# Kernel optimization log

Measured on AMD Instinct MI355X. Metric: run time of the kernel, lower is better.

## Reference

```python
import jax, jax.numpy as jnp
import numpy as np

N_NODES = 100000


def _mean_agg(x, src, dst, n_nodes):
    # gather source features along edges, segment-sum into destinations, divide by in-degree
    msg = x[src]                                               # [E, D]
    s = jax.ops.segment_sum(msg, dst, num_segments=n_nodes)    # [N, D]
    deg = jax.ops.segment_sum(jnp.ones((src.shape[0],), x.dtype), dst, num_segments=n_nodes)
    return s / jnp.maximum(deg, 1.0)[:, None]


def _sage_layer(x, src, dst, W_self, W_neigh, b, n_nodes):
    h_neigh = _mean_agg(x, src, dst, n_nodes)
    return x @ W_self + h_neigh @ W_neigh + b


def setup_inputs() -> dict:
    key = jax.random.key(0)
    ks = jax.random.split(key, 8)
    in_f, h_f, n_cls = 128, 128, 40
    n_edges = 1600000
    sc = lambda d: 1.0 / np.sqrt(d)
    return {
        "features": jax.random.normal(ks[0], (N_NODES, in_f), dtype=jnp.float32),
        "src": jax.random.randint(ks[1], (n_edges,), 0, N_NODES),
        "dst": jax.random.randint(ks[2], (n_edges,), 0, N_NODES),
        "W1_self": jax.random.normal(ks[3], (in_f, h_f), dtype=jnp.float32) * sc(in_f),
        "W1_neigh": jax.random.normal(ks[4], (in_f, h_f), dtype=jnp.float32) * sc(in_f),
        "b1": jnp.zeros((h_f,), dtype=jnp.float32),
        "W2_self": jax.random.normal(ks[5], (h_f, n_cls), dtype=jnp.float32) * sc(h_f),
        "W2_neigh": jax.random.normal(ks[6], (h_f, n_cls), dtype=jnp.float32) * sc(h_f),
        "b2": jnp.zeros((n_cls,), dtype=jnp.float32),
    }


def reference(features, src, dst, W1_self, W1_neigh, b1, W2_self, W2_neigh, b2):
    h = _sage_layer(features, src, dst, W1_self, W1_neigh, b1, N_NODES)
    h = jax.nn.relu(h)
    h = _sage_layer(h, src, dst, W2_self, W2_neigh, b2, N_NODES)
    return h
```

## Files before the change

kernel.cpp:

```cpp
#include <hip/hip_runtime.h>


typedef __attribute__((ext_vector_type(8))) short bf16x8;
typedef __attribute__((ext_vector_type(4))) float f32x4;

#define BIN_SHIFT 7
#define BIN_SIZE  128
#define NB        256

#define OFF_ROWSTART (1ull << 20)
#define OFF_HIST     (2ull << 20)
#define OFF_SCAN     (3ull << 20)
#define OFF_BSUMS    (4ull << 20)
#define OFF_BOFFS    ((4ull << 20) + (64ull << 10))
#define OFF_PACKED   (5ull << 20)
#define OFF_CSR      (12ull << 20)
#define OFF_W1T      (19ull << 20)
#define OFF_W2T      (20ull << 20)
#define OFF_XB       (21ull << 20)
#define OFF_AGGB     (47ull << 20)
#define OFF_T2LO     (73ull << 20)
#define OFF_T2HI     (80ull << 20)

static __device__ __forceinline__ unsigned short f2b(float f) {
    unsigned int u = __float_as_uint(f);
    u += 0x7fffu + ((u >> 16) & 1u);
    return (unsigned short)(u >> 16);
}
static __device__ __forceinline__ float blo(unsigned int v) { return __uint_as_float(v << 16); }
static __device__ __forceinline__ float bhi(unsigned int v) { return __uint_as_float(v & 0xffff0000u); }


__global__ __launch_bounds__(256) void hist_local(
    const int* __restrict__ dst, int* __restrict__ hist, int E, int nbins) {
    __shared__ int h[1024];
    int b = blockIdx.x, t = threadIdx.x;
    for (int i = t; i < nbins; i += 256) h[i] = 0;
    __syncthreads();
    int chunk = (E + NB - 1) / NB;
    int base = b * chunk;
    int lim = min(base + chunk, E);
    for (int e = base + t; e < lim; e += 256)
        atomicAdd(&h[dst[e] >> BIN_SHIFT], 1);
    __syncthreads();
    for (int i = t; i < nbins; i += 256)
        hist[i * NB + b] = h[i];
}

__global__ void scan1(const int* __restrict__ in, int* __restrict__ tmp,
                      int* __restrict__ bsums, int M) {
    __shared__ int s[256];
    int t = threadIdx.x;
    int i = blockIdx.x * 256 + t;
    int v = (i < M) ? in[i] : 0;
    s[t] = v;
    __syncthreads();
    for (int off = 1; off < 256; off <<= 1) {
        int u = (t >= off) ? s[t - off] : 0;
        __syncthreads();
        s[t] += u;
        __syncthreads();
    }
    if (i < M) tmp[i] = s[t] - v;
    if (t == 255) bsums[blockIdx.x] = s[t];
}

__global__ void scan2(const int* __restrict__ bsums, int* __restrict__ boffs, int nb) {
    __shared__ int s[1024];
    int t = threadIdx.x;
    int v = (t < nb) ? bsums[t] : 0;
    s[t] = v;
    __syncthreads();
    for (int off = 1; off < 1024; off <<= 1) {
        int u = (t >= off) ? s[t - off] : 0;
        __syncthreads();
        s[t] += u;
        __syncthreads();
    }
    if (t < nb) boffs[t] = s[t] - v;
}

__global__ void scan3(int* __restrict__ tmp, const int* __restrict__ boffs, int M) {
    int i = blockIdx.x * 256 + threadIdx.x;
    if (i < M) tmp[i] += boffs[blockIdx.x];
}

__global__ __launch_bounds__(256) void scatter_det(
    const int* __restrict__ src, const int* __restrict__ dst,
    const int* __restrict__ scanned, unsigned int* __restrict__ packed,
    int E, int nbins) {
    __shared__ int cur[1024];
    int b = blockIdx.x, t = threadIdx.x;
    for (int i = t; i < nbins; i += 256) cur[i] = scanned[i * NB + b];
    __syncthreads();
    int chunk = (E + NB - 1) / NB;
    int base = b * chunk;
    int lim = min(base + chunk, E);
    for (int e = base + t; e < lim; e += 256) {
        int d = dst[e];
        int bin = d >> BIN_SHIFT;
        int pos = atomicAdd(&cur[bin], 1);
        packed[pos] = ((unsigned int)(d & (BIN_SIZE - 1)) << 20) | (unsigned int)src[e];
    }
}

__global__ __launch_bounds__(256) void bin_fill(
    const unsigned int* __restrict__ packed, const int* __restrict__ scanned,
    int* __restrict__ row_start, int* __restrict__ csr_src, int N, int nbins, int E) {
    __shared__ int cnt[BIN_SIZE];
    __shared__ int pre[BIN_SIZE];
    __shared__ int ex[BIN_SIZE];
    int b = blockIdx.x;
    int t = threadIdx.x;
    int node0 = b << BIN_SHIFT;
    int beg = scanned[b * NB];
    int end = (b + 1 < nbins) ? scanned[(b + 1) * NB] : E;

    if (t < BIN_SIZE) cnt[t] = 0;
    __syncthreads();
    for (int i = beg + t; i < end; i += 256)
        atomicAdd(&cnt[packed[i] >> 20], 1);
    __syncthreads();
    if (t < BIN_SIZE) pre[t] = cnt[t];
    __syncthreads();
    for (int off = 1; off < BIN_SIZE; off <<= 1) {
        int u = (t < BIN_SIZE && t >= off) ? pre[t - off] : 0;
        __syncthreads();
        if (t < BIN_SIZE) pre[t] += u;
        __syncthreads();
    }
    if (t < BIN_SIZE) {
        ex[t] = pre[t] - cnt[t];
        int node = node0 + t;
        if (node < N) row_start[node] = beg + ex[t];
        cnt[t] = 0;
    }
    if (b == nbins - 1 && t == 0) row_start[N] = E;
    __syncthreads();
    for (int i = beg + t; i < end; i += 256) {
        unsigned int p = packed[i];
        int dl = p >> 20;
        int s = p & 0xFFFFF;
        int ofs = atomicAdd(&cnt[dl], 1);
        csr_src[beg + ex[dl] + ofs] = s;
    }
}


__global__ void cast_bf16(const float* __restrict__ x, unsigned short* __restrict__ xb, int n8) {
    int i = blockIdx.x * blockDim.x + threadIdx.x;
    if (i >= n8) return;
    const float4* p = (const float4*)x + (size_t)i * 2;
    float4 v0 = p[0], v1 = p[1];
    unsigned short o[8];
    o[0] = f2b(v0.x); o[1] = f2b(v0.y); o[2] = f2b(v0.z); o[3] = f2b(v0.w);
    o[4] = f2b(v1.x); o[5] = f2b(v1.y); o[6] = f2b(v1.z); o[7] = f2b(v1.w);
    *(float4*)(xb + (size_t)i * 8) = *(float4*)o;
}

__global__ void prep_weights(const float* __restrict__ W1s, const float* __restrict__ W1n,
                             const float* __restrict__ W2s, const float* __restrict__ W2n,
                             unsigned short* __restrict__ W1t, unsigned short* __restrict__ W2t) {
    int blk = blockIdx.x, k = threadIdx.x;
    if (blk < 128) {
        int c = blk;
        float v = (k < 128) ? W1s[(size_t)k * 128 + c] : W1n[(size_t)(k - 128) * 128 + c];
        W1t[(size_t)c * 256 + k] = f2b(v);
    } else if (k < 128) {
        int c = blk - 128;
        float v = (c < 40) ? W2s[(size_t)k * 40 + c] : W2n[(size_t)k * 40 + (c - 40)];
        W2t[(size_t)c * 128 + k] = f2b(v);
    }
}


__global__ void agg_mean_bf16(const unsigned short* __restrict__ xb,
                              const int* __restrict__ row_start,
                              const int* __restrict__ csr_src,
                              unsigned short* __restrict__ aggb, int N) {
    int wave = (blockIdx.x * blockDim.x + threadIdx.x) >> 6;
    int lane = threadIdx.x & 63;
    if (wave >= N) return;
    int q = lane >> 4;
    int l = lane & 15;
    int beg = row_start[wave], end = row_start[wave + 1];
    const char* xbase = (const char*)xb;
    unsigned loff = (unsigned)l << 4;

    float a0 = 0.f, a1 = 0.f, a2 = 0.f, a3 = 0.f;
    float a4 = 0.f, a5 = 0.f, a6 = 0.f, a7 = 0.f;

    int e = beg;
    for (; e + 16 <= end; e += 16) {
        int eq = e + 4 * q;
        int s0 = csr_src[eq + 0];
        int s1 = csr_src[eq + 1];
        int s2 = csr_src[eq + 2];
        int s3 = csr_src[eq + 3];
        uint4 v0 = *(const uint4*)(xbase + (((unsigned)s0 << 8) + loff));
        uint4 v1 = *(const uint4*)(xbase + (((unsigned)s1 << 8) + loff));
        uint4 v2 = *(const uint4*)(xbase + (((unsigned)s2 << 8) + loff));
        uint4 v3 = *(const uint4*)(xbase + (((unsigned)s3 << 8) + loff));
        a0 += blo(v0.x) + blo(v1.x) + blo(v2.x) + blo(v3.x);
        a1 += bhi(v0.x) + bhi(v1.x) + bhi(v2.x) + bhi(v3.x);
        a2 += blo(v0.y) + blo(v1.y) + blo(v2.y) + blo(v3.y);
        a3 += bhi(v0.y) + bhi(v1.y) + bhi(v2.y) + bhi(v3.y);
        a4 += blo(v0.z) + blo(v1.z) + blo(v2.z) + blo(v3.z);
        a5 += bhi(v0.z) + bhi(v1.z) + bhi(v2.z) + bhi(v3.z);
        a6 += blo(v0.w) + blo(v1.w) + blo(v2.w) + blo(v3.w);
        a7 += bhi(v0.w) + bhi(v1.w) + bhi(v2.w) + bhi(v3.w);
    }
    for (; e + 4 <= end; e += 4) {
        int s = csr_src[e + q];
        uint4 v = *(const uint4*)(xbase + (((unsigned)s << 8) + loff));
        a0 += blo(v.x); a1 += bhi(v.x); a2 += blo(v.y); a3 += bhi(v.y);
        a4 += blo(v.z); a5 += bhi(v.z); a6 += blo(v.w); a7 += bhi(v.w);
    }
    int rem = end - e;
    if (q < rem) {
        int s = csr_src[e + q];
        uint4 v = *(const uint4*)(xbase + (((unsigned)s << 8) + loff));
        a0 += blo(v.x); a1 += bhi(v.x); a2 += blo(v.y); a3 += bhi(v.y);
        a4 += blo(v.z); a5 += bhi(v.z); a6 += blo(v.w); a7 += bhi(v.w);
    }
    a0 += __shfl_xor(a0, 16); a0 += __shfl_xor(a0, 32);
    a1 += __shfl_xor(a1, 16); a1 += __shfl_xor(a1, 32);
    a2 += __shfl_xor(a2, 16); a2 += __shfl_xor(a2, 32);
    a3 += __shfl_xor(a3, 16); a3 += __shfl_xor(a3, 32);
    a4 += __shfl_xor(a4, 16); a4 += __shfl_xor(a4, 32);
    a5 += __shfl_xor(a5, 16); a5 += __shfl_xor(a5, 32);
    a6 += __shfl_xor(a6, 16); a6 += __shfl_xor(a6, 32);
    a7 += __shfl_xor(a7, 16); a7 += __shfl_xor(a7, 32);
    if (q == 0) {
        float inv = 1.0f / fmaxf((float)(end - beg), 1.0f);
        uint4 o;
        o.x = (unsigned int)f2b(a0 * inv) | ((unsigned int)f2b(a1 * inv) << 16);
        o.y = (unsigned int)f2b(a2 * inv) | ((unsigned int)f2b(a3 * inv) << 16);
        o.z = (unsigned int)f2b(a4 * inv) | ((unsigned int)f2b(a5 * inv) << 16);
        o.w = (unsigned int)f2b(a6 * inv) | ((unsigned int)f2b(a7 * inv) << 16);
        *(uint4*)((char*)aggb + (((unsigned)wave << 8) + loff)) = o;
    }
}

__global__ void agg2_add(const unsigned short* __restrict__ t2lo,
                         const unsigned short* __restrict__ t2hi,
                         const int* __restrict__ row_start,
                         const int* __restrict__ csr_src, const float* __restrict__ b2,
                         float* __restrict__ out, int N) {
    int wave = (blockIdx.x * blockDim.x + threadIdx.x) >> 6;
    int lane = threadIdx.x & 63;
    if (wave >= N) return;
    int q = lane >> 4;
    int l = lane & 15;
    int beg = row_start[wave], end = row_start[wave + 1];
    const char* lob = (const char*)t2lo;
    const char* hib = (const char*)t2hi;
    bool isLo = (l < 8);
    bool active = (l < 10);
    unsigned loff = isLo ? ((unsigned)l << 3) : ((unsigned)(l - 8) << 3);

    float a0 = 0.f, a1 = 0.f, a2 = 0.f, a3 = 0.f;

    int e = beg;
    for (; e + 16 <= end; e += 16) {
        int eq = e + 4 * q;
        int s0 = csr_src[eq + 0];
        int s1 = csr_src[eq + 1];
        int s2 = csr_src[eq + 2];
        int s3 = csr_src[eq + 3];
        if (active) {
            uint2 v0, v1, v2, v3;
            if (isLo) {
                v0 = *(const uint2*)(lob + (((unsigned)s0 << 6) + loff));
                v1 = *(const uint2*)(lob + (((unsigned)s1 << 6) + loff));
                v2 = *(const uint2*)(lob + (((unsigned)s2 << 6) + loff));
                v3 = *(const uint2*)(lob + (((unsigned)s3 << 6) + loff));
            } else {
                v0 = *(const uint2*)(hib + (((unsigned)s0 << 4) + loff));
                v1 = *(const uint2*)(hib + (((unsigned)s1 << 4) + loff));
                v2 = *(const uint2*)(hib + (((unsigned)s2 << 4) + loff));
                v3 = *(const uint2*)(hib + (((unsigned)s3 << 4) + loff));
            }
            a0 += blo(v0.x) + blo(v1.x) + blo(v2.x) + blo(v3.x);
            a1 += bhi(v0.x) + bhi(v1.x) + bhi(v2.x) + bhi(v3.x);
            a2 += blo(v0.y) + blo(v1.y) + blo(v2.y) + blo(v3.y);
            a3 += bhi(v0.y) + bhi(v1.y) + bhi(v2.y) + bhi(v3.y);
        }
    }
    for (; e + 4 <= end; e += 4) {
        int s = csr_src[e + q];
        if (active) {
            uint2 v = isLo ? *(const uint2*)(lob + (((unsigned)s << 6) + loff))
                           : *(const uint2*)(hib + (((unsigned)s << 4) + loff));
            a0 += blo(v.x); a1 += bhi(v.x); a2 += blo(v.y); a3 += bhi(v.y);
        }
    }
    int rem = end - e;
    if (q < rem) {
        int s = csr_src[e + q];
        if (active) {
            uint2 v = isLo ? *(const uint2*)(lob + (((unsigned)s << 6) + loff))
                           : *(const uint2*)(hib + (((unsigned)s << 4) + loff));
            a0 += blo(v.x); a1 += bhi(v.x); a2 += blo(v.y); a3 += bhi(v.y);
        }
    }
    a0 += __shfl_xor(a0, 16); a0 += __shfl_xor(a0, 32);
    a1 += __shfl_xor(a1, 16); a1 += __shfl_xor(a1, 32);
    a2 += __shfl_xor(a2, 16); a2 += __shfl_xor(a2, 32);
    a3 += __shfl_xor(a3, 16); a3 += __shfl_xor(a3, 32);
    if (q == 0 && active) {
        float inv = 1.0f / fmaxf((float)(end - beg), 1.0f);
        float4 bb = ((const float4*)b2)[l];
        float4* op = (float4*)((char*)out + ((unsigned)wave * 160u + ((unsigned)l << 4)));
        float4 cur = *op;
        cur.x += a0 * inv + bb.x;
        cur.y += a1 * inv + bb.y;
        cur.z += a2 * inv + bb.z;
        cur.w += a3 * inv + bb.w;
        *op = cur;
    }
}


__global__ __launch_bounds__(256) void gemm12_mfma(
    const unsigned short* __restrict__ xb, const unsigned short* __restrict__ aggb,
    const unsigned short* __restrict__ W1t, const unsigned short* __restrict__ W2t,
    const float* __restrict__ b1, float* __restrict__ out,
    unsigned short* __restrict__ t2lo, unsigned short* __restrict__ t2hi, int N) {

    __shared__ unsigned short As[128 * 40];
    __shared__ unsigned short Bs[128 * 40];
    __shared__ unsigned short Hs[128 * 136];
    __shared__ unsigned short B2[80 * 136];

    int tid = threadIdx.x;
    int wave = tid >> 6, lane = tid & 63;
    int row0 = blockIdx.x * 128;
    int m = lane & 15, quad = lane >> 4;

    for (int idx = tid; idx < 1280; idx += 256) {
        int r = idx >> 4, seg = idx & 15;
        *(float4*)&B2[r * 136 + seg * 8] = *(const float4*)(W2t + (size_t)r * 128 + seg * 8);
    }

    f32x4 acc[2][8];
#pragma unroll
    for (int i = 0; i < 2; i++)
#pragma unroll
        for (int j = 0; j < 8; j++) acc[i][j] = (f32x4){0.f, 0.f, 0.f, 0.f};

    for (int k0 = 0; k0 < 256; k0 += 32) {
        __syncthreads();
        {
            int r = tid >> 1, kk = (tid & 1) * 16;
            int row = row0 + r;
            float4 v0 = make_float4(0, 0, 0, 0), v1 = v0;
            if (row < N) {
                const unsigned short* s = (k0 < 128)
                    ? (xb + (size_t)row * 128 + k0 + kk)
                    : (aggb + (size_t)row * 128 + (k0 - 128) + kk);
                const float4* p = (const float4*)s;
                v0 = p[0]; v1 = p[1];
            }
            *(float4*)&As[r * 40 + kk] = v0;
            *(float4*)&As[r * 40 + kk + 8] = v1;
            const float4* q2 = (const float4*)(W1t + (size_t)r * 256 + k0 + kk);
            float4 w0 = q2[0], w1 = q2[1];
            *(float4*)&Bs[r * 40 + kk] = w0;
            *(float4*)&Bs[r * 40 + kk + 8] = w1;
        }
        __syncthreads();

        bf16x8 af0 = *(bf16x8*)&As[(wave * 32 + m) * 40 + quad * 8];
        bf16x8 af1 = *(bf16x8*)&As[(wave * 32 + 16 + m) * 40 + quad * 8];
#pragma unroll
        for (int j = 0; j < 8; j++) {
            bf16x8 bfg = *(bf16x8*)&Bs[(j * 16 + m) * 40 + quad * 8];
            acc[0][j] = __builtin_amdgcn_mfma_f32_16x16x32_bf16(af0, bfg, acc[0][j], 0, 0, 0);
            acc[1][j] = __builtin_amdgcn_mfma_f32_16x16x32_bf16(af1, bfg, acc[1][j], 0, 0, 0);
        }
    }

#pragma unroll
    for (int j = 0; j < 8; j++) {
        int col = j * 16 + m;
        float bias = b1[col];
#pragma unroll
        for (int i = 0; i < 2; i++) {
#pragma unroll
            for (int r = 0; r < 4; r++) {
                int rl = wave * 32 + i * 16 + quad * 4 + r;
                Hs[rl * 136 + col] = f2b(fmaxf(acc[i][j][r] + bias, 0.f));
            }
        }
    }
    __syncthreads();

    f32x4 acc2[2][5];
#pragma unroll
    for (int i = 0; i < 2; i++)
#pragma unroll
        for (int j = 0; j < 5; j++) acc2[i][j] = (f32x4){0.f, 0.f, 0.f, 0.f};

#pragma unroll
    for (int k0 = 0; k0 < 128; k0 += 32) {
        bf16x8 af0 = *(bf16x8*)&Hs[(wave * 32 + m) * 136 + k0 + quad * 8];
        bf16x8 af1 = *(bf16x8*)&Hs[(wave * 32 + 16 + m) * 136 + k0 + quad * 8];
#pragma unroll
        for (int j = 0; j < 5; j++) {
            bf16x8 bfg = *(bf16x8*)&B2[(j * 16 + m) * 136 + k0 + quad * 8];
            acc2[0][j] = __builtin_amdgcn_mfma_f32_16x16x32_bf16(af0, bfg, acc2[0][j], 0, 0, 0);
            acc2[1][j] = __builtin_amdgcn_mfma_f32_16x16x32_bf16(af1, bfg, acc2[1][j], 0, 0, 0);
        }
    }

#pragma unroll
    for (int j = 0; j < 5; j++) {
        int col = j * 16 + m;
#pragma unroll
        for (int i = 0; i < 2; i++) {
#pragma unroll
            for (int r = 0; r < 4; r++) {
                int row = row0 + wave * 32 + i * 16 + quad * 4 + r;
                if (row < N) {
                    float v = acc2[i][j][r];
                    if (col < 40) {
                        out[(size_t)row * 40 + col] = v;
                    } else {
                        int td = col - 40;
                        if (td < 32) t2lo[(size_t)row * 32 + td] = f2b(v);
                        else         t2hi[(size_t)row * 8 + (td - 32)] = f2b(v);
                    }
                }
            }
        }
    }
}


extern "C" void kernel_launch(void* const* d_in, const int* in_sizes, int n_in,
                              void* d_out, int out_size, void* d_ws, size_t ws_size,
                              hipStream_t stream) {
    const float* x   = (const float*)d_in[0];
    const int*   src = (const int*)d_in[1];
    const int*   dst = (const int*)d_in[2];
    const float* W1s = (const float*)d_in[3];
    const float* W1n = (const float*)d_in[4];
    const float* b1  = (const float*)d_in[5];
    const float* W2s = (const float*)d_in[6];
    const float* W2n = (const float*)d_in[7];
    const float* b2  = (const float*)d_in[8];
    float* out = (float*)d_out;

    int N = in_sizes[0] / 128;
    int E = in_sizes[1];
    int nbins = (N + BIN_SIZE - 1) / BIN_SIZE;
    int M = nbins * NB;

    char* ws = (char*)d_ws;
    int*            row_start  = (int*)(ws + OFF_ROWSTART);
    int*            hist       = (int*)(ws + OFF_HIST);
    int*            scanned    = (int*)(ws + OFF_SCAN);
    int*            bsums      = (int*)(ws + OFF_BSUMS);
    int*            boffs      = (int*)(ws + OFF_BOFFS);
    unsigned int*   packed     = (unsigned int*)(ws + OFF_PACKED);
    int*            csr_src    = (int*)(ws + OFF_CSR);
    unsigned short* W1t        = (unsigned short*)(ws + OFF_W1T);
    unsigned short* W2t        = (unsigned short*)(ws + OFF_W2T);
    unsigned short* xb         = (unsigned short*)(ws + OFF_XB);
    unsigned short* aggb       = (unsigned short*)(ws + OFF_AGGB);
    unsigned short* t2lo       = (unsigned short*)(ws + OFF_T2LO);
    unsigned short* t2hi       = (unsigned short*)(ws + OFF_T2HI);

    int scanBlocks = (M + 255) / 256;

    hist_local<<<NB, 256, 0, stream>>>(dst, hist, E, nbins);
    scan1<<<scanBlocks, 256, 0, stream>>>(hist, scanned, bsums, M);
    scan2<<<1, 1024, 0, stream>>>(bsums, boffs, scanBlocks);
    scan3<<<scanBlocks, 256, 0, stream>>>(scanned, boffs, M);
    scatter_det<<<NB, 256, 0, stream>>>(src, dst, scanned, packed, E, nbins);
    bin_fill<<<nbins, 256, 0, stream>>>(packed, scanned, row_start, csr_src, N, nbins, E);

    int n8 = N * 128 / 8;
    cast_bf16<<<(n8 + 255) / 256, 256, 0, stream>>>(x, xb, n8);
    prep_weights<<<208, 256, 0, stream>>>(W1s, W1n, W2s, W2n, W1t, W2t);

    int aggBlocks = (N * 64 + 255) / 256;
    agg_mean_bf16<<<aggBlocks, 256, 0, stream>>>(xb, row_start, csr_src, aggb, N);
    gemm12_mfma<<<(N + 127) / 128, 256, 0, stream>>>(xb, aggb, W1t, W2t, b1, out, t2lo, t2hi, N);
    agg2_add<<<aggBlocks, 256, 0, stream>>>(t2lo, t2hi, row_start, csr_src, b2, out, N);
}
```

Measured before the change: 306.9 us.

## Gather layer-1 neighbor features in FP8 and fold scan3 and cast kernels

Adds an FP8 (e4m3) copy of the input features, produced alongside the bf16 cast, and switches the first-layer mean aggregation to gather 128-byte FP8 rows instead of 256-byte bf16 rows. This halves the random-gather traffic that dominates that kernel. It also drops the scan3 kernel by adding the block offsets inline in scatter/bin_fill, and merges the cast and weight-prep kernels into one launch. The FP8 quantization of features lowers the accuracy of the neighbor mean and risks exceeding the tolerance.

```diff
diff --git a/kernel.cpp b/kernel.cpp
--- a/kernel.cpp
+++ b/kernel.cpp
@@ -3,6 +3,7 @@
 
 typedef __attribute__((ext_vector_type(8))) short bf16x8;
 typedef __attribute__((ext_vector_type(4))) float f32x4;
+typedef __attribute__((ext_vector_type(2))) float f32x2;
 
 #define BIN_SHIFT 7
 #define BIN_SIZE  128
@@ -18,9 +19,10 @@
 #define OFF_W1T      (19ull << 20)
 #define OFF_W2T      (20ull << 20)
 #define OFF_XB       (21ull << 20)
-#define OFF_AGGB     (47ull << 20)
-#define OFF_T2LO     (73ull << 20)
-#define OFF_T2HI     (80ull << 20)
+#define OFF_XQ       (47ull << 20)
+#define OFF_AGGB     (61ull << 20)
+#define OFF_T2LO     (87ull << 20)
+#define OFF_T2HI     (94ull << 20)
 
 static __device__ __forceinline__ unsigned short f2b(float f) {
     unsigned int u = __float_as_uint(f);
@@ -80,18 +82,13 @@
     if (t < nb) boffs[t] = s[t] - v;
 }
 
-__global__ void scan3(int* __restrict__ tmp, const int* __restrict__ boffs, int M) {
-    int i = blockIdx.x * 256 + threadIdx.x;
-    if (i < M) tmp[i] += boffs[blockIdx.x];
-}
-
 __global__ __launch_bounds__(256) void scatter_det(
     const int* __restrict__ src, const int* __restrict__ dst,
-    const int* __restrict__ scanned, unsigned int* __restrict__ packed,
-    int E, int nbins) {
+    const int* __restrict__ tmp, const int* __restrict__ boffs,
+    unsigned int* __restrict__ packed, int E, int nbins) {
     __shared__ int cur[1024];
     int b = blockIdx.x, t = threadIdx.x;
-    for (int i = t; i < nbins; i += 256) cur[i] = scanned[i * NB + b];
+    for (int i = t; i < nbins; i += 256) cur[i] = tmp[i * NB + b] + boffs[i];
     __syncthreads();
     int chunk = (E + NB - 1) / NB;
     int base = b * chunk;
@@ -105,7 +102,8 @@
 }
 
 __global__ __launch_bounds__(256) void bin_fill(
-    const unsigned int* __restrict__ packed, const int* __restrict__ scanned,
+    const unsigned int* __restrict__ packed, const int* __restrict__ tmp,
+    const int* __restrict__ boffs,
     int* __restrict__ row_start, int* __restrict__ csr_src, int N, int nbins, int E) {
     __shared__ int cnt[BIN_SIZE];
     __shared__ int pre[BIN_SIZE];
@@ -113,8 +111,8 @@
     int b = blockIdx.x;
     int t = threadIdx.x;
     int node0 = b << BIN_SHIFT;
-    int beg = scanned[b * NB];
-    int end = (b + 1 < nbins) ? scanned[(b + 1) * NB] : E;
+    int beg = tmp[b * NB] + boffs[b];
+    int end = (b + 1 < nbins) ? (tmp[(b + 1) * NB] + boffs[b + 1]) : E;
 
     if (t < BIN_SIZE) cnt[t] = 0;
     __syncthreads();
@@ -147,98 +145,112 @@
 }
 
 
-__global__ void cast_bf16(const float* __restrict__ x, unsigned short* __restrict__ xb, int n8) {
-    int i = blockIdx.x * blockDim.x + threadIdx.x;
-    if (i >= n8) return;
-    const float4* p = (const float4*)x + (size_t)i * 2;
-    float4 v0 = p[0], v1 = p[1];
-    unsigned short o[8];
-    o[0] = f2b(v0.x); o[1] = f2b(v0.y); o[2] = f2b(v0.z); o[3] = f2b(v0.w);
-    o[4] = f2b(v1.x); o[5] = f2b(v1.y); o[6] = f2b(v1.z); o[7] = f2b(v1.w);
-    *(float4*)(xb + (size_t)i * 8) = *(float4*)o;
-}
-
-__global__ void prep_weights(const float* __restrict__ W1s, const float* __restrict__ W1n,
-                             const float* __restrict__ W2s, const float* __restrict__ W2n,
-                             unsigned short* __restrict__ W1t, unsigned short* __restrict__ W2t) {
-    int blk = blockIdx.x, k = threadIdx.x;
-    if (blk < 128) {
-        int c = blk;
-        float v = (k < 128) ? W1s[(size_t)k * 128 + c] : W1n[(size_t)(k - 128) * 128 + c];
-        W1t[(size_t)c * 256 + k] = f2b(v);
-    } else if (k < 128) {
-        int c = blk - 128;
-        float v = (c < 40) ? W2s[(size_t)k * 40 + c] : W2n[(size_t)k * 40 + (c - 40)];
-        W2t[(size_t)c * 128 + k] = f2b(v);
-    }
-}
-
-
-__global__ void agg_mean_bf16(const unsigned short* __restrict__ xb,
-                              const int* __restrict__ row_start,
-                              const int* __restrict__ csr_src,
-                              unsigned short* __restrict__ aggb, int N) {
+__global__ void cast_prep(const float* __restrict__ x,
+                          const float* __restrict__ W1s, const float* __restrict__ W1n,
+                          const float* __restrict__ W2s, const float* __restrict__ W2n,
+                          unsigned short* __restrict__ xb, unsigned char* __restrict__ xq,
+                          unsigned short* __restrict__ W1t, unsigned short* __restrict__ W2t,
+                          int n16, int castBlocks) {
+    int blk = blockIdx.x, t = threadIdx.x;
+    if (blk < castBlocks) {
+        int i = blk * 256 + t;
+        if (i >= n16) return;
+        const float4* p = (const float4*)x + (size_t)i * 4;
+        float4 v0 = p[0], v1 = p[1], v2 = p[2], v3 = p[3];
+        float f[16] = {v0.x, v0.y, v0.z, v0.w, v1.x, v1.y, v1.z, v1.w,
+                       v2.x, v2.y, v2.z, v2.w, v3.x, v3.y, v3.z, v3.w};
+        unsigned short ob[16];
+#pragma unroll
+        for (int k = 0; k < 16; k++) ob[k] = f2b(f[k]);
+        *(float4*)(xb + (size_t)i * 16) = *(float4*)&ob[0];
+        *(float4*)(xb + (size_t)i * 16 + 8) = *(float4*)&ob[8];
+        unsigned int w[4];
+#pragma unroll
+        for (int k = 0; k < 4; k++) {
+            int u = __builtin_amdgcn_cvt_pk_fp8_f32(f[4 * k + 0], f[4 * k + 1], 0, false);
+            u = __builtin_amdgcn_cvt_pk_fp8_f32(f[4 * k + 2], f[4 * k + 3], u, true);
+            w[k] = (unsigned int)u;
+        }
+        *(uint4*)(xq + (size_t)i * 16) = *(uint4*)w;
+    } else if (blk < castBlocks + 128) {
+        int c = blk - castBlocks;
+        float v = (t < 128) ? W1s[(size_t)t * 128 + c] : W1n[(size_t)(t - 128) * 128 + c];
+        W1t[(size_t)c * 256 + t] = f2b(v);
+    } else if (t < 128) {
+        int c = blk - castBlocks - 128;
+        float v = (c < 40) ? W2s[(size_t)t * 40 + c] : W2n[(size_t)t * 40 + (c - 40)];
+        W2t[(size_t)c * 128 + t] = f2b(v);
+    }
+}
+
+
+__global__ void agg_mean_fp8(const unsigned char* __restrict__ xq,
+                             const int* __restrict__ row_start,
+                             const int* __restrict__ csr_src,
+                             unsigned short* __restrict__ aggb, int N) {
     int wave = (blockIdx.x * blockDim.x + threadIdx.x) >> 6;
     int lane = threadIdx.x & 63;
     if (wave >= N) return;
-    int q = lane >> 4;
-    int l = lane & 15;
+    int g = lane >> 3;
+    int l = lane & 7;
     int beg = row_start[wave], end = row_start[wave + 1];
-    const char* xbase = (const char*)xb;
+    const char* xbase = (const char*)xq;
     unsigned loff = (unsigned)l << 4;
 
-    float a0 = 0.f, a1 = 0.f, a2 = 0.f, a3 = 0.f;
-    float a4 = 0.f, a5 = 0.f, a6 = 0.f, a7 = 0.f;
+    float a[16];
+#pragma unroll
+    for (int k = 0; k < 16; k++) a[k] = 0.f;
+
+#define ACC16(V)                                                        \
+    {                                                                   \
+        unsigned int wd[4] = {(V).x, (V).y, (V).z, (V).w};              \
+        _Pragma("unroll")                                               \
+        for (int k = 0; k < 4; k++) {                                   \
+            f32x2 p0 = __builtin_amdgcn_cvt_pk_f32_fp8(wd[k], false);   \
+            f32x2 p1 = __builtin_amdgcn_cvt_pk_f32_fp8(wd[k], true);    \
+            a[4 * k + 0] += p0.x; a[4 * k + 1] += p0.y;                 \
+            a[4 * k + 2] += p1.x; a[4 * k + 3] += p1.y;                 \
+        }                                                               \
+    }
 
     int e = beg;
     for (; e + 16 <= end; e += 16) {
-        int eq = e + 4 * q;
-        int s0 = csr_src[eq + 0];
-        int s1 = csr_src[eq + 1];
-        int s2 = csr_src[eq + 2];
-        int s3 = csr_src[eq + 3];
-        uint4 v0 = *(const uint4*)(xbase + (((unsigned)s0 << 8) + loff));
-        uint4 v1 = *(const uint4*)(xbase + (((unsigned)s1 << 8) + loff));
-        uint4 v2 = *(const uint4*)(xbase + (((unsigned)s2 << 8) + loff));
-        uint4 v3 = *(const uint4*)(xbase + (((unsigned)s3 << 8) + loff));
-        a0 += blo(v0.x) + blo(v1.x) + blo(v2.x) + blo(v3.x);
-        a1 += bhi(v0.x) + bhi(v1.x) + bhi(v2.x) + bhi(v3.x);
-        a2 += blo(v0.y) + blo(v1.y) + blo(v2.y) + blo(v3.y);
-        a3 += bhi(v0.y) + bhi(v1.y) + bhi(v2.y) + bhi(v3.y);
-        a4 += blo(v0.z) + blo(v1.z) + blo(v2.z) + blo(v3.z);
-        a5 += bhi(v0.z) + bhi(v1.z) + bhi(v2.z) + bhi(v3.z);
-        a6 += blo(v0.w) + blo(v1.w) + blo(v2.w) + blo(v3.w);
-        a7 += bhi(v0.w) + bhi(v1.w) + bhi(v2.w) + bhi(v3.w);
-    }
-    for (; e + 4 <= end; e += 4) {
-        int s = csr_src[e + q];
-        uint4 v = *(const uint4*)(xbase + (((unsigned)s << 8) + loff));
-        a0 += blo(v.x); a1 += bhi(v.x); a2 += blo(v.y); a3 += bhi(v.y);
-        a4 += blo(v.z); a5 += bhi(v.z); a6 += blo(v.w); a7 += bhi(v.w);
+        int s0 = csr_src[e + g];
+        int s1 = csr_src[e + 8 + g];
+        uint4 v0 = *(const uint4*)(xbase + (((unsigned)s0 << 7) + loff));
+        uint4 v1 = *(const uint4*)(xbase + (((unsigned)s1 << 7) + loff));
+        ACC16(v0);
+        ACC16(v1);
+    }
+    for (; e + 8 <= end; e += 8) {
+        int s = csr_src[e + g];
+        uint4 v = *(const uint4*)(xbase + (((unsigned)s << 7) + loff));
+        ACC16(v);
     }
     int rem = end - e;
-    if (q < rem) {
-        int s = csr_src[e + q];
-        uint4 v = *(const uint4*)(xbase + (((unsigned)s << 8) + loff));
-        a0 += blo(v.x); a1 += bhi(v.x); a2 += blo(v.y); a3 += bhi(v.y);
-        a4 += blo(v.z); a5 += bhi(v.z); a6 += blo(v.w); a7 += bhi(v.w);
-    }
-    a0 += __shfl_xor(a0, 16); a0 += __shfl_xor(a0, 32);
-    a1 += __shfl_xor(a1, 16); a1 += __shfl_xor(a1, 32);
-    a2 += __shfl_xor(a2, 16); a2 += __shfl_xor(a2, 32);
-    a3 += __shfl_xor(a3, 16); a3 += __shfl_xor(a3, 32);
-    a4 += __shfl_xor(a4, 16); a4 += __shfl_xor(a4, 32);
-    a5 += __shfl_xor(a5, 16); a5 += __shfl_xor(a5, 32);
-    a6 += __shfl_xor(a6, 16); a6 += __shfl_xor(a6, 32);
-    a7 += __shfl_xor(a7, 16); a7 += __shfl_xor(a7, 32);
-    if (q == 0) {
+    if (g < rem) {
+        int s = csr_src[e + g];
+        uint4 v = *(const uint4*)(xbase + (((unsigned)s << 7) + loff));
+        ACC16(v);
+    }
+#undef ACC16
+
+#pragma unroll
+    for (int k = 0; k < 16; k++) {
+        a[k] += __shfl_xor(a[k], 8);
+        a[k] += __shfl_xor(a[k], 16);
+        a[k] += __shfl_xor(a[k], 32);
+    }
+    if (g == 0) {
         float inv = 1.0f / fmaxf((float)(end - beg), 1.0f);
-        uint4 o;
-        o.x = (unsigned int)f2b(a0 * inv) | ((unsigned int)f2b(a1 * inv) << 16);
-        o.y = (unsigned int)f2b(a2 * inv) | ((unsigned int)f2b(a3 * inv) << 16);
-        o.z = (unsigned int)f2b(a4 * inv) | ((unsigned int)f2b(a5 * inv) << 16);
-        o.w = (unsigned int)f2b(a6 * inv) | ((unsigned int)f2b(a7 * inv) << 16);
-        *(uint4*)((char*)aggb + (((unsigned)wave << 8) + loff)) = o;
+        unsigned int ow[8];
+#pragma unroll
+        for (int k = 0; k < 8; k++)
+            ow[k] = (unsigned int)f2b(a[2 * k] * inv) |
+                    ((unsigned int)f2b(a[2 * k + 1] * inv) << 16);
+        char* obase = (char*)aggb + (((unsigned)wave << 8) + ((unsigned)l << 5));
+        *(uint4*)obase = *(uint4*)&ow[0];
+        *(uint4*)(obase + 16) = *(uint4*)&ow[4];
     }
 }
 
@@ -468,6 +480,7 @@
     unsigned short* W1t        = (unsigned short*)(ws + OFF_W1T);
     unsigned short* W2t        = (unsigned short*)(ws + OFF_W2T);
     unsigned short* xb         = (unsigned short*)(ws + OFF_XB);
+    unsigned char*  xq         = (unsigned char*)(ws + OFF_XQ);
     unsigned short* aggb       = (unsigned short*)(ws + OFF_AGGB);
     unsigned short* t2lo       = (unsigned short*)(ws + OFF_T2LO);
     unsigned short* t2hi       = (unsigned short*)(ws + OFF_T2HI);
@@ -477,16 +490,16 @@
     hist_local<<<NB, 256, 0, stream>>>(dst, hist, E, nbins);
     scan1<<<scanBlocks, 256, 0, stream>>>(hist, scanned, bsums, M);
     scan2<<<1, 1024, 0, stream>>>(bsums, boffs, scanBlocks);
-    scan3<<<scanBlocks, 256, 0, stream>>>(scanned, boffs, M);
-    scatter_det<<<NB, 256, 0, stream>>>(src, dst, scanned, packed, E, nbins);
-    bin_fill<<<nbins, 256, 0, stream>>>(packed, scanned, row_start, csr_src, N, nbins, E);
-
-    int n8 = N * 128 / 8;
-    cast_bf16<<<(n8 + 255) / 256, 256, 0, stream>>>(x, xb, n8);
-    prep_weights<<<208, 256, 0, stream>>>(W1s, W1n, W2s, W2n, W1t, W2t);
+    scatter_det<<<NB, 256, 0, stream>>>(src, dst, scanned, boffs, packed, E, nbins);
+    bin_fill<<<nbins, 256, 0, stream>>>(packed, scanned, boffs, row_start, csr_src, N, nbins, E);
+
+    int n16 = N * 128 / 16;
+    int castBlocks = (n16 + 255) / 256;
+    cast_prep<<<castBlocks + 128 + 80, 256, 0, stream>>>(
+        x, W1s, W1n, W2s, W2n, xb, xq, W1t, W2t, n16, castBlocks);
 
     int aggBlocks = (N * 64 + 255) / 256;
-    agg_mean_bf16<<<aggBlocks, 256, 0, stream>>>(xb, row_start, csr_src, aggb, N);
+    agg_mean_fp8<<<aggBlocks, 256, 0, stream>>>(xq, row_start, csr_src, aggb, N);
     gemm12_mfma<<<(N + 127) / 128, 256, 0, stream>>>(xb, aggb, W1t, W2t, b1, out, t2lo, t2hi, N);
     agg2_add<<<aggBlocks, 256, 0, stream>>>(t2lo, t2hi, row_start, csr_src, b2, out, N);
 }
```

New measurement: 294.9 us. 1.04x faster.
